# Kernel optimization log

Measured on AMD Instinct MI355X. Metric: run time of the kernel, lower is better.

## Reference

```python
import jax
jax.config.update("jax_enable_x64", True)
import jax.numpy as jnp
import numpy as np

INPUT_DIM = 2048
NUM_BINS = 32
RMS_EPS = 1e-4  # RunningMeanStd initial count


def setup_inputs() -> dict:
    key = jax.random.key(0)
    k1, k2 = jax.random.split(key)
    features = jax.random.normal(k1, (64, 256, INPUT_DIM), dtype=jnp.float32)
    # register_buffer: randn(input_dim, num_bins) / sqrt(input_dim)
    random_projection = jax.random.normal(k2, (INPUT_DIM, NUM_BINS), dtype=jnp.float32) / np.sqrt(INPUT_DIM)
    return {"features": features, "random_projection": random_projection}


def _occurrence_counts(keys):
    """For each element, 1 + number of earlier elements with the same key.
    Stable argsort keeps original order inside each duplicate run, so the
    rank within a run equals the sequential visit count."""
    n = keys.shape[0]
    order = jnp.argsort(keys)  # stable
    sk = keys[order]
    idx = jnp.arange(n, dtype=jnp.int64)
    new_run = jnp.concatenate([jnp.ones((1,), bool), sk[1:] != sk[:-1]])
    starts = jax.lax.cummax(jnp.where(new_run, idx, 0))
    counts_sorted = idx - starts + 1
    return jnp.zeros(n, jnp.int64).at[order].set(counts_sorted)


def reference(features, random_projection):
    batch, seq, feat = features.shape
    x = features.reshape(-1, feat)
    n = x.shape[0]

    # RunningMeanStd.update from fresh state (mean=0, var=1, count=1e-4)
    bm = jnp.mean(x, axis=0)
    bv = jnp.var(x, axis=0, ddof=1)  # torch .var(dim=0) is unbiased
    tot = RMS_EPS + n
    mean = bm * (n / tot)  # delta = bm - 0
    m2 = 1.0 * RMS_EPS + bv * n + (bm ** 2) * (RMS_EPS * n / tot)
    var = m2 / tot
    sigma = jnp.sqrt(var + 1e-8)

    normalized = (x - mean) / sigma
    projected = normalized @ random_projection  # [n, num_bins]
    bits = (projected > 0).astype(jnp.int64)
    powers = (2 ** jnp.arange(min(NUM_BINS, 63), dtype=jnp.int64))
    h = (bits[:, : powers.shape[0]] * powers).sum(axis=-1)  # < 2^32

    env = jnp.arange(n, dtype=jnp.int64) % batch  # default env_indices path
    keys = h * batch + env  # unique per (env, hash), fits int64
    counts = _occurrence_counts(keys)

    rewards = 1.0 / jnp.sqrt(counts.astype(features.dtype))
    return rewards.reshape(batch, seq, 1)
```

## Files before the change

### kernel.cpp

```cpp
#include <hip/hip_runtime.h>
#include <math.h>

#define FEAT 2048
#define NBINS 32
#define NROWS 16384
#define NCLS 64
#define SB 1024
#define RPB 16

typedef __attribute__((ext_vector_type(8))) short short8;
typedef __attribute__((ext_vector_type(4))) float f32x4;

static __device__ __forceinline__ unsigned int pk2bf(float a, float b) {
    unsigned ua = __float_as_uint(a);
    unsigned ub = __float_as_uint(b);
    ua = (ua + 0x7FFFu + ((ua >> 16) & 1u)) >> 16;
    ub = (ub + 0x7FFFu + ((ub >> 16) & 1u)) & 0xFFFF0000u;
    return ua | ub;
}

__global__ __launch_bounds__(256) void k1_stats(const float* __restrict__ x,
                                                float* __restrict__ pS1,
                                                float* __restrict__ pS2) {
    const int b = blockIdx.x, t = threadIdx.x;
    const float4* xb = reinterpret_cast<const float4*>(x) + (size_t)b * RPB * (FEAT / 4);
    float4 s1a = make_float4(0.f,0.f,0.f,0.f), s1b = make_float4(0.f,0.f,0.f,0.f);
    float4 s2a = make_float4(0.f,0.f,0.f,0.f), s2b = make_float4(0.f,0.f,0.f,0.f);
    #pragma unroll
    for (int r = 0; r < RPB; ++r) {
        const float4 va = xb[(size_t)r * (FEAT / 4) + t];
        const float4 vb = xb[(size_t)r * (FEAT / 4) + t + 256];
        s1a.x += va.x; s1a.y += va.y; s1a.z += va.z; s1a.w += va.w;
        s2a.x += va.x * va.x; s2a.y += va.y * va.y; s2a.z += va.z * va.z; s2a.w += va.w * va.w;
        s1b.x += vb.x; s1b.y += vb.y; s1b.z += vb.z; s1b.w += vb.w;
        s2b.x += vb.x * vb.x; s2b.y += vb.y * vb.y; s2b.z += vb.z * vb.z; s2b.w += vb.w * vb.w;
    }
    float4* o1 = reinterpret_cast<float4*>(pS1 + (size_t)b * FEAT);
    float4* o2 = reinterpret_cast<float4*>(pS2 + (size_t)b * FEAT);
    o1[t] = s1a; o1[t + 256] = s1b;
    o2[t] = s2a; o2[t + 256] = s2b;
}

__global__ __launch_bounds__(256) void k2_stats(const float* __restrict__ pS1,
                                                const float* __restrict__ pS2,
                                                float* __restrict__ ms,
                                                float* __restrict__ isig_g) {
    __shared__ double sh1[32][8];
    __shared__ double sh2[32][8];
    const int t = threadIdx.x;
    const int ci = t & 7, s = t >> 3;
    const int c = blockIdx.x * 8 + ci;
    double S1 = 0.0, S2 = 0.0;
    #pragma unroll 4
    for (int j = 0; j < 32; ++j) {
        const int k = s * 32 + j;
        S1 += (double)pS1[(size_t)k * FEAT + c];
        S2 += (double)pS2[(size_t)k * FEAT + c];
    }
    sh1[s][ci] = S1; sh2[s][ci] = S2;
    __syncthreads();
    if (t < 8) {
        double s1 = 0.0, s2 = 0.0;
        #pragma unroll
        for (int q = 0; q < 32; ++q) { s1 += sh1[q][t]; s2 += sh2[q][t]; }
        const int cc = blockIdx.x * 8 + t;
        const double n = (double)NROWS;
        const double bm = s1 / n;
        const double bv = (s2 - s1 * s1 / n) / (n - 1.0);
        const double tot = 1e-4 + n;
        const double mean = bm * (n / tot);
        const double m2 = 1e-4 + bv * n + bm * bm * (1e-4 * n / tot);
        const double var = m2 / tot;
        const double isig = 1.0 / sqrt(var + 1e-8);
        ms[cc] = (float)(mean * isig);
        isig_g[cc] = (float)isig;
    }
}

__global__ __launch_bounds__(256) void k2_misc(const float* __restrict__ isig_g,
                                               const float* __restrict__ ms,
                                               const float* __restrict__ P,
                                               unsigned int* __restrict__ QTf,
                                               float* __restrict__ offs) {
    const int t = threadIdx.x;
    if (blockIdx.x < 64) {
        __shared__ float isig_sh[32];
        if (t < 32) isig_sh[t] = isig_g[blockIdx.x * 32 + t];
        __syncthreads();
        const int nb = t >> 7;
        const int lane = (t & 127) >> 1;
        const int half = t & 1;
        const int lrow = lane & 15, lk = lane >> 4;
        const int bin = nb * 16 + lrow;
        const int ccl = lk * 8 + half * 4;
        const int cc = blockIdx.x * 32 + ccl;
        unsigned int w0 = pk2bf(P[(size_t)cc * NBINS + bin] * isig_sh[ccl],
                                P[(size_t)(cc + 1) * NBINS + bin] * isig_sh[ccl + 1]);
        unsigned int w1 = pk2bf(P[(size_t)(cc + 2) * NBINS + bin] * isig_sh[ccl + 2],
                                P[(size_t)(cc + 3) * NBINS + bin] * isig_sh[ccl + 3]);
        const int ch = blockIdx.x >> 2, ks = blockIdx.x & 3;
        char* dst = reinterpret_cast<char*>(QTf) +
                    (size_t)(((nb * 16 + ch) * 4 + ks) * 1024 + lane * 16 + half * 8);
        uint2 pk; pk.x = w0; pk.y = w1;
        *reinterpret_cast<uint2*>(dst) = pk;
    } else {
        __shared__ double sh[256];
        const int b = blockIdx.x - 64;
        double s = 0.0;
        for (int f = t; f < FEAT; f += 256) s += (double)ms[f] * (double)P[(size_t)f * NBINS + b];
        sh[t] = s;
        __syncthreads();
        for (int st = 128; st > 0; st >>= 1) {
            if (t < st) sh[t] += sh[t + st];
            __syncthreads();
        }
        if (t == 0) offs[b] = (float)sh[0];
    }
}

__global__ __launch_bounds__(256, 1) void k3_mfma(const float* __restrict__ x,
                                                  const unsigned int* __restrict__ QTf,
                                                  const float* __restrict__ offs,
                                                  unsigned int* __restrict__ hout) {
    const int t = threadIdx.x;
    const int w = t >> 6, l = t & 63;
    const int lrow = l & 15, lk = l >> 4;
    const int bid = blockIdx.x;

    const float* ax = x + (size_t)(bid * 64 + w * 16 + lrow) * FEAT + lk * 8;
    const short8* b0p = reinterpret_cast<const short8*>(QTf) + l;
    const short8* b1p = b0p + 4096;

    f32x4 acc0 = {0.f, 0.f, 0.f, 0.f};
    f32x4 acc1 = {0.f, 0.f, 0.f, 0.f};

    float4 va[8], vb[8];
    short8 b0s[8], b1s[8];

    #pragma unroll
    for (int p = 0; p < 8; ++p) {
        va[p] = *reinterpret_cast<const float4*>(ax + p * 32);
        vb[p] = *reinterpret_cast<const float4*>(ax + p * 32 + 4);
        b0s[p] = b0p[p * 64];
        b1s[p] = b1p[p * 64];
    }

    const float* axg = ax;
    const short8* b0g = b0p;
    const short8* b1g = b1p;
    #pragma unroll 1
    for (int g = 0; g < 7; ++g) {
        #pragma unroll
        for (int s2 = 0; s2 < 8; ++s2) {
            uint4 ap;
            ap.x = pk2bf(va[s2].x, va[s2].y); ap.y = pk2bf(va[s2].z, va[s2].w);
            ap.z = pk2bf(vb[s2].x, vb[s2].y); ap.w = pk2bf(vb[s2].z, vb[s2].w);
            const short8 a = __builtin_bit_cast(short8, ap);
            acc0 = __builtin_amdgcn_mfma_f32_16x16x32_bf16(a, b0s[s2], acc0, 0, 0, 0);
            acc1 = __builtin_amdgcn_mfma_f32_16x16x32_bf16(a, b1s[s2], acc1, 0, 0, 0);
            va[s2] = *reinterpret_cast<const float4*>(axg + (8 + s2) * 32);
            vb[s2] = *reinterpret_cast<const float4*>(axg + (8 + s2) * 32 + 4);
            b0s[s2] = b0g[(8 + s2) * 64];
            b1s[s2] = b1g[(8 + s2) * 64];
        }
        axg += 256; b0g += 512; b1g += 512;
    }
    #pragma unroll
    for (int s2 = 0; s2 < 8; ++s2) {
        uint4 ap;
        ap.x = pk2bf(va[s2].x, va[s2].y); ap.y = pk2bf(va[s2].z, va[s2].w);
        ap.z = pk2bf(vb[s2].x, vb[s2].y); ap.w = pk2bf(vb[s2].z, vb[s2].w);
        const short8 a = __builtin_bit_cast(short8, ap);
        acc0 = __builtin_amdgcn_mfma_f32_16x16x32_bf16(a, b0s[s2], acc0, 0, 0, 0);
        acc1 = __builtin_amdgcn_mfma_f32_16x16x32_bf16(a, b1s[s2], acc1, 0, 0, 0);
    }

    const float o0 = offs[lrow];
    const float o1 = offs[16 + lrow];
    #pragma unroll
    for (int r = 0; r < 4; ++r) {
        const unsigned long long m0 = __ballot(acc0[r] > o0);
        const unsigned long long m1 = __ballot(acc1[r] > o1);
        if (lrow == 0) {
            const unsigned int h =
                (unsigned int)((m0 >> (16 * lk)) & 0xFFFFull) |
                ((unsigned int)((m1 >> (16 * lk)) & 0xFFFFull) << 16);
            const int irow = w * 16 + lk * 4 + r;
            hout[(size_t)irow * 256 + bid] = h;
        }
    }
}

__global__ __launch_bounds__(256) void k4_count(const unsigned int* __restrict__ hcls,
                                                float* __restrict__ out) {
    __shared__ unsigned int hh[256];
    const int c = blockIdx.x, t = threadIdx.x;
    hh[t] = hcls[(size_t)c * 256 + t];
    __syncthreads();
    const unsigned int mine = hh[t];
    int cnt = 1;
    for (int j = 0; j < 256; ++j) {
        cnt += (j < t && hh[j] == mine) ? 1 : 0;
    }
    out[(size_t)t * NCLS + c] = 1.0f / sqrtf((float)cnt);
}

extern "C" void kernel_launch(void* const* d_in, const int* in_sizes, int n_in,
                              void* d_out, int out_size, void* d_ws, size_t ws_size,
                              hipStream_t stream) {
    const float* x = (const float*)d_in[0];
    const float* P = (const float*)d_in[1];
    float* out = (float*)d_out;
    char* ws = (char*)d_ws;

    float* pS1 = (float*)(ws);
    float* pS2 = (float*)(ws + (size_t)SB * FEAT * 4);
    float* ms  = (float*)(ws + (size_t)16 * 1024 * 1024);
    float* isig = ms + FEAT;
    float* offsB = isig + FEAT;
    unsigned int* QTf = (unsigned int*)(ws + (size_t)17 * 1024 * 1024);
    unsigned int* h   = (unsigned int*)(ws + (size_t)18 * 1024 * 1024);

    k1_stats<<<SB, 256, 0, stream>>>(x, pS1, pS2);
    k2_stats<<<256, 256, 0, stream>>>(pS1, pS2, ms, isig);
    k2_misc<<<96, 256, 0, stream>>>(isig, ms, P, QTf, offsB);
    k3_mfma<<<256, 256, 0, stream>>>(x, QTf, offsB, h);
    k4_count<<<NCLS, 256, 0, stream>>>(h, out);
}
```

Measured before the change: 70.40 us.

## Split K across waves in projection kernel and double stats partial blocks

The projection kernel now gives each block 16 rows instead of 64. Its four waves each cover a quarter of the feature dimension, and the partial MFMA accumulators are reduced through shared memory before the hash ballot. This raises the grid from 256 to 1024 blocks and shortens each wave's prefetch pipeline, aiming to fill more CUs and hide memory latency better. The stats kernel likewise uses twice as many blocks with half the rows each. The cost is an extra LDS reduction and sync, a larger partial-sum workspace, and more partial rows for the second stats pass to read.

```diff
diff --git a/kernel.cpp b/kernel.cpp
--- a/kernel.cpp
+++ b/kernel.cpp
@@ -5,8 +5,8 @@
 #define NBINS 32
 #define NROWS 16384
 #define NCLS 64
-#define SB 1024
-#define RPB 16
+#define SB 2048
+#define RPB 8
 
 typedef __attribute__((ext_vector_type(8))) short short8;
 typedef __attribute__((ext_vector_type(4))) float f32x4;
@@ -19,9 +19,9 @@
     return ua | ub;
 }
 
-__global__ __launch_bounds__(256) void k1_stats(const float* __restrict__ x,
-                                                float* __restrict__ pS1,
-                                                float* __restrict__ pS2) {
+__global__ __launch_bounds__(256, 8) void k1_stats(const float* __restrict__ x,
+                                                   float* __restrict__ pS1,
+                                                   float* __restrict__ pS2) {
     const int b = blockIdx.x, t = threadIdx.x;
     const float4* xb = reinterpret_cast<const float4*>(x) + (size_t)b * RPB * (FEAT / 4);
     float4 s1a = make_float4(0.f,0.f,0.f,0.f), s1b = make_float4(0.f,0.f,0.f,0.f);
@@ -52,8 +52,8 @@
     const int c = blockIdx.x * 8 + ci;
     double S1 = 0.0, S2 = 0.0;
     #pragma unroll 4
-    for (int j = 0; j < 32; ++j) {
-        const int k = s * 32 + j;
+    for (int j = 0; j < (SB / 32); ++j) {
+        const int k = s * (SB / 32) + j;
         S1 += (double)pS1[(size_t)k * FEAT + c];
         S2 += (double)pS2[(size_t)k * FEAT + c];
     }
@@ -118,75 +118,82 @@
     }
 }
 
-__global__ __launch_bounds__(256, 1) void k3_mfma(const float* __restrict__ x,
+__global__ __launch_bounds__(256, 4) void k3_mfma(const float* __restrict__ x,
                                                   const unsigned int* __restrict__ QTf,
                                                   const float* __restrict__ offs,
                                                   unsigned int* __restrict__ hout) {
+    __shared__ f32x4 red[3][2][64];
     const int t = threadIdx.x;
     const int w = t >> 6, l = t & 63;
     const int lrow = l & 15, lk = l >> 4;
     const int bid = blockIdx.x;
-
-    const float* ax = x + (size_t)(bid * 64 + w * 16 + lrow) * FEAT + lk * 8;
-    const short8* b0p = reinterpret_cast<const short8*>(QTf) + l;
-    const short8* b1p = b0p + 4096;
+    const int tile = bid >> 2, q = bid & 3;
+
+    const float* ax = x + (size_t)(bid * 16 + lrow) * FEAT + w * 512 + lk * 8;
+    const short8* b0g = reinterpret_cast<const short8*>(QTf) + l + (w * 16) * 64;
+    const short8* b1g = b0g + 4096;
 
     f32x4 acc0 = {0.f, 0.f, 0.f, 0.f};
     f32x4 acc1 = {0.f, 0.f, 0.f, 0.f};
 
-    float4 va[8], vb[8];
-    short8 b0s[8], b1s[8];
-
+    float4 va[4], vb[4];
+    short8 b0s[4], b1s[4];
     #pragma unroll
-    for (int p = 0; p < 8; ++p) {
+    for (int p = 0; p < 4; ++p) {
         va[p] = *reinterpret_cast<const float4*>(ax + p * 32);
         vb[p] = *reinterpret_cast<const float4*>(ax + p * 32 + 4);
-        b0s[p] = b0p[p * 64];
-        b1s[p] = b1p[p * 64];
+        b0s[p] = b0g[p * 64];
+        b1s[p] = b1g[p * 64];
     }
 
     const float* axg = ax;
-    const short8* b0g = b0p;
-    const short8* b1g = b1p;
+    const short8* bb0 = b0g;
+    const short8* bb1 = b1g;
     #pragma unroll 1
-    for (int g = 0; g < 7; ++g) {
+    for (int g = 0; g < 3; ++g) {
         #pragma unroll
-        for (int s2 = 0; s2 < 8; ++s2) {
-            uint4 ap;
-            ap.x = pk2bf(va[s2].x, va[s2].y); ap.y = pk2bf(va[s2].z, va[s2].w);
-            ap.z = pk2bf(vb[s2].x, vb[s2].y); ap.w = pk2bf(vb[s2].z, vb[s2].w);
-            const short8 a = __builtin_bit_cast(short8, ap);
+        for (int s2 = 0; s2 < 4; ++s2) {
+            uint4 apk;
+            apk.x = pk2bf(va[s2].x, va[s2].y); apk.y = pk2bf(va[s2].z, va[s2].w);
+            apk.z = pk2bf(vb[s2].x, vb[s2].y); apk.w = pk2bf(vb[s2].z, vb[s2].w);
+            const short8 a = __builtin_bit_cast(short8, apk);
             acc0 = __builtin_amdgcn_mfma_f32_16x16x32_bf16(a, b0s[s2], acc0, 0, 0, 0);
             acc1 = __builtin_amdgcn_mfma_f32_16x16x32_bf16(a, b1s[s2], acc1, 0, 0, 0);
-            va[s2] = *reinterpret_cast<const float4*>(axg + (8 + s2) * 32);
-            vb[s2] = *reinterpret_cast<const float4*>(axg + (8 + s2) * 32 + 4);
-            b0s[s2] = b0g[(8 + s2) * 64];
-            b1s[s2] = b1g[(8 + s2) * 64];
+            va[s2] = *reinterpret_cast<const float4*>(axg + (4 + s2) * 32);
+            vb[s2] = *reinterpret_cast<const float4*>(axg + (4 + s2) * 32 + 4);
+            b0s[s2] = bb0[(4 + s2) * 64];
+            b1s[s2] = bb1[(4 + s2) * 64];
         }
-        axg += 256; b0g += 512; b1g += 512;
+        axg += 128; bb0 += 256; bb1 += 256;
     }
     #pragma unroll
-    for (int s2 = 0; s2 < 8; ++s2) {
-        uint4 ap;
-        ap.x = pk2bf(va[s2].x, va[s2].y); ap.y = pk2bf(va[s2].z, va[s2].w);
-        ap.z = pk2bf(vb[s2].x, vb[s2].y); ap.w = pk2bf(vb[s2].z, vb[s2].w);
-        const short8 a = __builtin_bit_cast(short8, ap);
+    for (int s2 = 0; s2 < 4; ++s2) {
+        uint4 apk;
+        apk.x = pk2bf(va[s2].x, va[s2].y); apk.y = pk2bf(va[s2].z, va[s2].w);
+        apk.z = pk2bf(vb[s2].x, vb[s2].y); apk.w = pk2bf(vb[s2].z, vb[s2].w);
+        const short8 a = __builtin_bit_cast(short8, apk);
         acc0 = __builtin_amdgcn_mfma_f32_16x16x32_bf16(a, b0s[s2], acc0, 0, 0, 0);
         acc1 = __builtin_amdgcn_mfma_f32_16x16x32_bf16(a, b1s[s2], acc1, 0, 0, 0);
     }
 
-    const float o0 = offs[lrow];
-    const float o1 = offs[16 + lrow];
-    #pragma unroll
-    for (int r = 0; r < 4; ++r) {
-        const unsigned long long m0 = __ballot(acc0[r] > o0);
-        const unsigned long long m1 = __ballot(acc1[r] > o1);
-        if (lrow == 0) {
-            const unsigned int h =
-                (unsigned int)((m0 >> (16 * lk)) & 0xFFFFull) |
-                ((unsigned int)((m1 >> (16 * lk)) & 0xFFFFull) << 16);
-            const int irow = w * 16 + lk * 4 + r;
-            hout[(size_t)irow * 256 + bid] = h;
+    if (w) { red[w - 1][0][l] = acc0; red[w - 1][1][l] = acc1; }
+    __syncthreads();
+    if (w == 0) {
+        acc0 += red[0][0][l]; acc0 += red[1][0][l]; acc0 += red[2][0][l];
+        acc1 += red[0][1][l]; acc1 += red[1][1][l]; acc1 += red[2][1][l];
+        const float o0 = offs[lrow];
+        const float o1 = offs[16 + lrow];
+        #pragma unroll
+        for (int r = 0; r < 4; ++r) {
+            const unsigned long long m0 = __ballot(acc0[r] > o0);
+            const unsigned long long m1 = __ballot(acc1[r] > o1);
+            if (lrow == 0) {
+                const unsigned int h =
+                    (unsigned int)((m0 >> (16 * lk)) & 0xFFFFull) |
+                    ((unsigned int)((m1 >> (16 * lk)) & 0xFFFFull) << 16);
+                const int cls = q * 16 + lk * 4 + r;
+                hout[(size_t)cls * 256 + tile] = h;
+            }
         }
     }
 }
@@ -215,15 +222,15 @@
 
     float* pS1 = (float*)(ws);
     float* pS2 = (float*)(ws + (size_t)SB * FEAT * 4);
-    float* ms  = (float*)(ws + (size_t)16 * 1024 * 1024);
+    float* ms  = (float*)(ws + (size_t)32 * 1024 * 1024);
     float* isig = ms + FEAT;
     float* offsB = isig + FEAT;
-    unsigned int* QTf = (unsigned int*)(ws + (size_t)17 * 1024 * 1024);
-    unsigned int* h   = (unsigned int*)(ws + (size_t)18 * 1024 * 1024);
+    unsigned int* QTf = (unsigned int*)(ws + (size_t)33 * 1024 * 1024);
+    unsigned int* h   = (unsigned int*)(ws + (size_t)34 * 1024 * 1024);
 
     k1_stats<<<SB, 256, 0, stream>>>(x, pS1, pS2);
     k2_stats<<<256, 256, 0, stream>>>(pS1, pS2, ms, isig);
     k2_misc<<<96, 256, 0, stream>>>(isig, ms, P, QTf, offsB);
-    k3_mfma<<<256, 256, 0, stream>>>(x, QTf, offsB, h);
+    k3_mfma<<<1024, 256, 0, stream>>>(x, QTf, offsB, h);
     k4_count<<<NCLS, 256, 0, stream>>>(h, out);
 }
```

Measured after the change: 91.00 us. +29.3%, slower.
